# Optimization experiments

Measured on AMD Instinct MI355X. Metric: run time of the kernel, lower is better.

## Reference

```python
import jax, jax.numpy as jnp
import numpy as np

D = 256  # in_channels == out_channels -> output_proj is Identity


def setup_inputs() -> dict:
    key = jax.random.key(0)
    ks = jax.random.split(key, 7)
    B, N = 4, 4096
    s = 1.0 / np.sqrt(D)
    return {
        "x": jax.random.normal(ks[0], (B, N, D), dtype=jnp.float32),
        "Wk": jax.random.normal(ks[1], (D, D), dtype=jnp.float32) * s,
        "bk": jax.random.normal(ks[2], (D,), dtype=jnp.float32) * 0.01,
        "Wq": jax.random.normal(ks[3], (D, D), dtype=jnp.float32) * s,
        "bq": jax.random.normal(ks[4], (D,), dtype=jnp.float32) * 0.01,
        "Wv": jax.random.normal(ks[5], (D, D), dtype=jnp.float32) * s,
        "bv": jax.random.normal(ks[6], (D,), dtype=jnp.float32) * 0.01,
    }


def reference(x, Wk, bk, Wq, bq, Wv, bv):
    # Linear projections: torch Linear(x) = x @ W.T + b; here W is stored as [in, out]
    keys = jnp.einsum("bnd,de->bne", x, Wk) + bk
    queries = jnp.einsum("bnd,de->bne", x, Wq) + bq
    values = jnp.einsum("bnd,de->bne", x, Wv) + bv
    scale = 1.0 / jnp.sqrt(jnp.float32(D))
    scores = jnp.einsum("bqd,bkd->bqk", queries, keys) * scale  # [B, N, N]
    attn = jax.nn.softmax(scores, axis=-1)
    out = jnp.einsum("bqk,bkd->bqd", attn, values)
    return out
```

## Files before the change

kernel.cpp:

```cpp
#include <hip/hip_runtime.h>
#include <hip/hip_bf16.h>


typedef __attribute__((ext_vector_type(8))) short bf16x8;
typedef __attribute__((ext_vector_type(4))) float f32x4;

__device__ __forceinline__ float b2f(ushort u){
  union { uint i; float f; } v; v.i = ((uint)u) << 16; return v.f;
}
__device__ __forceinline__ ushort f2b(float f){
  union { float f; uint i; } v; v.f = f;
  uint i = v.i;
  return (ushort)((i + 0x7FFFu + ((i >> 16) & 1u)) >> 16);
}
__device__ __forceinline__ uint pack2(float a, float b){
  return (uint)f2b(a) | ((uint)f2b(b) << 16);
}

#define Q_SCALE 0.0901684400555602f
#define FIXED_M 16.0f

__global__ __launch_bounds__(256) void transpose_w_kernel(
    const float* __restrict__ Wk, const float* __restrict__ Wq,
    const float* __restrict__ Wv, ushort* __restrict__ Wt){
  __shared__ ushort t[64][72];
  const float* src = (blockIdx.y == 0) ? Wk : (blockIdx.y == 1) ? Wq : Wv;
  ushort* dst = Wt + blockIdx.y * 65536;
  int tile = blockIdx.x;
  int tr = tile >> 2, tc = tile & 3;
  int tid = threadIdx.x;
  for (int i = tid; i < 1024; i += 256){
    int r = i >> 4, ch = i & 15;
    float4 f = *(const float4*)(src + (tr*64 + r)*256 + tc*64 + ch*4);
    uint2 u; u.x = pack2(f.x, f.y); u.y = pack2(f.z, f.w);
    *(uint2*)&t[r][ch*4] = u;
  }
  __syncthreads();
  for (int i = tid; i < 2048; i += 256){
    int c = i >> 5, r2 = (i & 31)*2;
    uint v = (uint)t[r2][c] | ((uint)t[r2+1][c] << 16);
    *(uint*)(dst + (tc*64 + c)*256 + tr*64 + r2) = v;
  }
}

__global__ __launch_bounds__(256) void proj_kernel(
    const float* __restrict__ x, const ushort* __restrict__ Wt,
    const float* __restrict__ bK, const float* __restrict__ bQ,
    const float* __restrict__ bV,
    ushort* __restrict__ Ko, ushort* __restrict__ Qo, ushort* __restrict__ Vt){
  __shared__ ushort xs[64][264];
  __shared__ ushort wt[16][264];
  int my = blockIdx.y;
  int n0 = blockIdx.x * 64;
  const ushort* wsrc = Wt + my*65536;
  const float* bias  = (my==0) ? bK : (my==1) ? bQ : bV;

  int tid = threadIdx.x;
  int lane = tid & 63, w = tid >> 6, quad = lane >> 4, l16 = lane & 15;

  for (int i = tid; i < 4096; i += 256){
    int r = i >> 6, ch = i & 63;
    float4 f = *(const float4*)(x + (size_t)(n0 + r)*256 + ch*4);
    uint2 u; u.x = pack2(f.x, f.y); u.y = pack2(f.z, f.w);
    *(uint2*)&xs[r][ch*4] = u;
  }
  __syncthreads();

  bf16x8 afr[8];
  #pragma unroll
  for (int ks = 0; ks < 8; ks++)
    afr[ks] = *(const bf16x8*)&xs[w*16 + l16][ks*32 + quad*8];

  for (int nt = 0; nt < 16; nt++){
    __syncthreads();
    for (int i = tid; i < 512; i += 256){
      int r = i >> 5, ch = i & 31;
      *(uint4*)&wt[r][ch*8] = *(const uint4*)(wsrc + (nt*16 + r)*256 + ch*8);
    }
    __syncthreads();
    f32x4 acc = {0.f, 0.f, 0.f, 0.f};
    #pragma unroll
    for (int ks = 0; ks < 8; ks++){
      bf16x8 bfr = *(const bf16x8*)&wt[l16][ks*32 + quad*8];
      acc = __builtin_amdgcn_mfma_f32_16x16x32_bf16(afr[ks], bfr, acc, 0, 0, 0);
    }
    int e = nt*16 + l16;
    float bv = bias[e];
    if (my == 2){
      int b  = n0 >> 12;
      int nl = (n0 & 4095) + w*16 + quad*4;
      ushort* vb = Vt + (size_t)b*1048576 + (size_t)e*4096 + nl;
      #pragma unroll
      for (int r = 0; r < 4; r++) vb[r] = f2b(acc[r] + bv);
    } else {
      float scale = (my==1) ? Q_SCALE : 1.0f;
      ushort* out = (my==0) ? Ko : Qo;
      #pragma unroll
      for (int r = 0; r < 4; r++){
        int row = n0 + w*16 + quad*4 + r;
        out[(size_t)row*256 + e] = f2b((acc[r] + bv) * scale);
      }
    }
  }
}

__global__ __launch_bounds__(256, 2) void attn_kernel(
    const ushort* __restrict__ Q, const ushort* __restrict__ K,
    const ushort* __restrict__ Vt,
    float* __restrict__ O0, ushort* __restrict__ Obf, float* __restrict__ lp){
  __shared__ ushort Ks[32][264];
  __shared__ ushort Vs[256][40];
  __shared__ ushort Ps[128][40];

  int bx   = blockIdx.x;
  int bh   = bx & 15;
  int b    = bh >> 2;
  int half = bh & 3;
  int qt   = bx >> 4;
  int tid = threadIdx.x, lane = tid & 63, w = tid >> 6;
  int quad = lane >> 4, l16 = lane & 15;

  const ushort* Qb = Q  + (size_t)(b*4096 + qt*128)*256;
  const ushort* Kb = K  + (size_t)b*4096*256;
  const ushort* Vb = Vt + (size_t)b*256*4096;

  bf16x8 qf[2][8];
  #pragma unroll
  for (int s = 0; s < 2; s++)
    #pragma unroll
    for (int ks = 0; ks < 8; ks++)
      qf[s][ks] = *(const bf16x8*)(Qb + (size_t)(w*32 + s*16 + l16)*256 + ks*32 + quad*8);

  f32x4 of[2][16];
  #pragma unroll
  for (int s = 0; s < 2; s++)
    #pragma unroll
    for (int dt = 0; dt < 16; dt++) of[s][dt] = (f32x4){0.f, 0.f, 0.f, 0.f};
  float l_i[2][4];
  #pragma unroll
  for (int s = 0; s < 2; s++)
    #pragma unroll
    for (int r = 0; r < 4; r++) l_i[s][r] = 0.f;

  int kt0 = half * 32;
  for (int kt = kt0; kt < kt0 + 32; kt++){
    __syncthreads();
    for (int i = tid; i < 1024; i += 256){
      int r = i >> 5, ch = i & 31;
      *(uint4*)&Ks[r][ch*8] = *(const uint4*)(Kb + (size_t)(kt*32 + r)*256 + ch*8);
    }
    for (int i = tid; i < 1024; i += 256){
      int d = i >> 2, ch = i & 3;
      *(uint4*)&Vs[d][ch*8] = *(const uint4*)(Vb + (size_t)d*4096 + kt*32 + ch*8);
    }
    __syncthreads();

    f32x4 sf[2][2];
    #pragma unroll
    for (int s = 0; s < 2; s++)
      #pragma unroll
      for (int nt = 0; nt < 2; nt++) sf[s][nt] = (f32x4){0.f, 0.f, 0.f, 0.f};
    #pragma unroll
    for (int nt = 0; nt < 2; nt++)
      #pragma unroll
      for (int ks = 0; ks < 8; ks++){
        bf16x8 bfr = *(const bf16x8*)&Ks[nt*16 + l16][ks*32 + quad*8];
        sf[0][nt] = __builtin_amdgcn_mfma_f32_16x16x32_bf16(qf[0][ks], bfr, sf[0][nt], 0,0,0);
        sf[1][nt] = __builtin_amdgcn_mfma_f32_16x16x32_bf16(qf[1][ks], bfr, sf[1][nt], 0,0,0);
      }

    #pragma unroll
    for (int s = 0; s < 2; s++){
      #pragma unroll
      for (int r = 0; r < 4; r++){
        float p0 = exp2f(sf[s][0][r] - FIXED_M);
        float p1 = exp2f(sf[s][1][r] - FIXED_M);
        l_i[s][r] += p0 + p1;
        Ps[w*32 + s*16 + quad*4 + r][l16]      = f2b(p0);
        Ps[w*32 + s*16 + quad*4 + r][16 + l16] = f2b(p1);
      }
    }
    __threadfence_block();

    bf16x8 pf0 = *(const bf16x8*)&Ps[w*32 +      l16][quad*8];
    bf16x8 pf1 = *(const bf16x8*)&Ps[w*32 + 16 + l16][quad*8];
    #pragma unroll
    for (int dt = 0; dt < 16; dt++){
      bf16x8 vf = *(const bf16x8*)&Vs[dt*16 + l16][quad*8];
      of[0][dt] = __builtin_amdgcn_mfma_f32_16x16x32_bf16(pf0, vf, of[0][dt], 0, 0, 0);
      of[1][dt] = __builtin_amdgcn_mfma_f32_16x16x32_bf16(pf1, vf, of[1][dt], 0, 0, 0);
    }
  }

  #pragma unroll
  for (int s = 0; s < 2; s++)
    #pragma unroll
    for (int r = 0; r < 4; r++){
      float rs = l_i[s][r];
      #pragma unroll
      for (int msk = 1; msk < 16; msk <<= 1) rs += __shfl_xor(rs, msk, 16);
      l_i[s][r] = rs;
    }

  #pragma unroll
  for (int s = 0; s < 2; s++){
    int gq0 = b*4096 + qt*128 + w*32 + s*16 + quad*4;
    if (l16 == 0){
      #pragma unroll
      for (int r = 0; r < 4; r++)
        lp[(size_t)half*16384 + gq0 + r] = l_i[s][r];
    }
    if (half == 0){
      #pragma unroll
      for (int dt = 0; dt < 16; dt++)
        #pragma unroll
        for (int r = 0; r < 4; r++)
          O0[(size_t)(gq0 + r)*256 + dt*16 + l16] = of[s][dt][r];
    } else {
      ushort* Oh = Obf + (size_t)(half - 1)*16384*256;
      #pragma unroll
      for (int dt = 0; dt < 16; dt++)
        #pragma unroll
        for (int r = 0; r < 4; r++)
          Oh[(size_t)(gq0 + r)*256 + dt*16 + l16] = f2b(of[s][dt][r]);
    }
  }
}

__global__ __launch_bounds__(256) void merge_kernel(
    float* __restrict__ O0, const ushort* __restrict__ Obf,
    const float* __restrict__ lp){
  int t   = blockIdx.x*256 + threadIdx.x;
  int row = t >> 6;
  int c   = (t & 63) * 4;
  float den = lp[row] + lp[16384 + row] + lp[2*16384 + row] + lp[3*16384 + row];
  float rden = 1.0f / den;
  size_t idx = (size_t)row*256 + c;
  float4 acc = *(float4*)&O0[idx];
  #pragma unroll
  for (int h = 1; h < 4; h++){
    ushort4 oh = *(const ushort4*)&Obf[(size_t)(h-1)*16384*256 + idx];
    acc.x += b2f(oh.x); acc.y += b2f(oh.y);
    acc.z += b2f(oh.z); acc.w += b2f(oh.w);
  }
  acc.x *= rden; acc.y *= rden; acc.z *= rden; acc.w *= rden;
  *(float4*)&O0[idx] = acc;
}

extern "C" void kernel_launch(void* const* d_in, const int* in_sizes, int n_in,
                              void* d_out, int out_size, void* d_ws, size_t ws_size,
                              hipStream_t stream){
  const float* x  = (const float*)d_in[0];
  const float* Wk = (const float*)d_in[1];
  const float* bk = (const float*)d_in[2];
  const float* Wq = (const float*)d_in[3];
  const float* bq = (const float*)d_in[4];
  const float* Wv = (const float*)d_in[5];
  const float* bv = (const float*)d_in[6];

  char* ws = (char*)d_ws;
  ushort* Wt  = (ushort*)(ws);
  ushort* Qb  = (ushort*)(ws + (size_t)1*(1u<<20));
  ushort* Kb  = (ushort*)(ws + (size_t)10*(1u<<20));
  ushort* Vtb = (ushort*)(ws + (size_t)19*(1u<<20));
  ushort* Obf = (ushort*)(ws + (size_t)28*(1u<<20));
  float*  lp  = (float*)(ws + (size_t)54*(1u<<20));

  hipLaunchKernelGGL(transpose_w_kernel, dim3(16, 3), dim3(256), 0, stream,
                     Wk, Wq, Wv, Wt);
  hipLaunchKernelGGL(proj_kernel, dim3(256, 3), dim3(256), 0, stream,
                     x, Wt, bk, bq, bv, Kb, Qb, Vtb);
  hipLaunchKernelGGL(attn_kernel, dim3(512), dim3(256), 0, stream,
                     Qb, Kb, Vtb, (float*)d_out, Obf, lp);
  hipLaunchKernelGGL(merge_kernel, dim3(4096), dim3(256), 0, stream,
                     (float*)d_out, Obf, lp);
}
```

Baseline: 237.8 us.

## Split attention KV range six ways, raise occupancy, read proj weights from global

The key range of the attention kernel is now split across six blocks per query tile instead of four. The grid grows to 768 blocks and launch bounds are raised to three blocks per CU, which should fill the 256-CU device more evenly. The projection kernel drops its shared-memory weight staging and the two barriers per tile, reading B fragments straight from global memory instead. The cost is more partial outputs to write and merge, more register pressure under the tighter launch bound, and uncoalesced or repeated weight reads in the projection.

```diff
diff --git a/kernel.cpp b/kernel.cpp
--- a/kernel.cpp
+++ b/kernel.cpp
@@ -19,6 +19,7 @@
 
 #define Q_SCALE 0.0901684400555602f
 #define FIXED_M 16.0f
+#define NSPLIT  6
 
 __global__ __launch_bounds__(256) void transpose_w_kernel(
     const float* __restrict__ Wk, const float* __restrict__ Wq,
@@ -49,7 +50,6 @@
     const float* __restrict__ bV,
     ushort* __restrict__ Ko, ushort* __restrict__ Qo, ushort* __restrict__ Vt){
   __shared__ ushort xs[64][264];
-  __shared__ ushort wt[16][264];
   int my = blockIdx.y;
   int n0 = blockIdx.x * 64;
   const ushort* wsrc = Wt + my*65536;
@@ -72,16 +72,10 @@
     afr[ks] = *(const bf16x8*)&xs[w*16 + l16][ks*32 + quad*8];
 
   for (int nt = 0; nt < 16; nt++){
-    __syncthreads();
-    for (int i = tid; i < 512; i += 256){
-      int r = i >> 5, ch = i & 31;
-      *(uint4*)&wt[r][ch*8] = *(const uint4*)(wsrc + (nt*16 + r)*256 + ch*8);
-    }
-    __syncthreads();
     f32x4 acc = {0.f, 0.f, 0.f, 0.f};
     #pragma unroll
     for (int ks = 0; ks < 8; ks++){
-      bf16x8 bfr = *(const bf16x8*)&wt[l16][ks*32 + quad*8];
+      bf16x8 bfr = *(const bf16x8*)(wsrc + (size_t)(nt*16 + l16)*256 + ks*32 + quad*8);
       acc = __builtin_amdgcn_mfma_f32_16x16x32_bf16(afr[ks], bfr, acc, 0, 0, 0);
     }
     int e = nt*16 + l16;
@@ -104,7 +98,7 @@
   }
 }
 
-__global__ __launch_bounds__(256, 2) void attn_kernel(
+__global__ __launch_bounds__(256, 3) void attn_kernel(
     const ushort* __restrict__ Q, const ushort* __restrict__ K,
     const ushort* __restrict__ Vt,
     float* __restrict__ O0, ushort* __restrict__ Obf, float* __restrict__ lp){
@@ -113,10 +107,10 @@
   __shared__ ushort Ps[128][40];
 
   int bx   = blockIdx.x;
-  int bh   = bx & 15;
-  int b    = bh >> 2;
-  int half = bh & 3;
-  int qt   = bx >> 4;
+  int bh   = bx % 24;
+  int b    = bh / NSPLIT;
+  int h    = bh % NSPLIT;
+  int qt   = bx / 24;
   int tid = threadIdx.x, lane = tid & 63, w = tid >> 6;
   int quad = lane >> 4, l16 = lane & 15;
 
@@ -142,8 +136,8 @@
     #pragma unroll
     for (int r = 0; r < 4; r++) l_i[s][r] = 0.f;
 
-  int kt0 = half * 32;
-  for (int kt = kt0; kt < kt0 + 32; kt++){
+  int kt0 = (h*128)/NSPLIT, kt1 = ((h+1)*128)/NSPLIT;
+  for (int kt = kt0; kt < kt1; kt++){
     __syncthreads();
     for (int i = tid; i < 1024; i += 256){
       int r = i >> 5, ch = i & 31;
@@ -208,16 +202,16 @@
     if (l16 == 0){
       #pragma unroll
       for (int r = 0; r < 4; r++)
-        lp[(size_t)half*16384 + gq0 + r] = l_i[s][r];
-    }
-    if (half == 0){
+        lp[(size_t)h*16384 + gq0 + r] = l_i[s][r];
+    }
+    if (h == 0){
       #pragma unroll
       for (int dt = 0; dt < 16; dt++)
         #pragma unroll
         for (int r = 0; r < 4; r++)
           O0[(size_t)(gq0 + r)*256 + dt*16 + l16] = of[s][dt][r];
     } else {
-      ushort* Oh = Obf + (size_t)(half - 1)*16384*256;
+      ushort* Oh = Obf + (size_t)(h - 1)*16384*256;
       #pragma unroll
       for (int dt = 0; dt < 16; dt++)
         #pragma unroll
@@ -233,12 +227,14 @@
   int t   = blockIdx.x*256 + threadIdx.x;
   int row = t >> 6;
   int c   = (t & 63) * 4;
-  float den = lp[row] + lp[16384 + row] + lp[2*16384 + row] + lp[3*16384 + row];
+  float den = 0.f;
+  #pragma unroll
+  for (int h = 0; h < NSPLIT; h++) den += lp[(size_t)h*16384 + row];
   float rden = 1.0f / den;
   size_t idx = (size_t)row*256 + c;
   float4 acc = *(float4*)&O0[idx];
   #pragma unroll
-  for (int h = 1; h < 4; h++){
+  for (int h = 1; h < NSPLIT; h++){
     ushort4 oh = *(const ushort4*)&Obf[(size_t)(h-1)*16384*256 + idx];
     acc.x += b2f(oh.x); acc.y += b2f(oh.y);
     acc.z += b2f(oh.z); acc.w += b2f(oh.w);
@@ -261,16 +257,16 @@
   char* ws = (char*)d_ws;
   ushort* Wt  = (ushort*)(ws);
   ushort* Qb  = (ushort*)(ws + (size_t)1*(1u<<20));
-  ushort* Kb  = (ushort*)(ws + (size_t)10*(1u<<20));
-  ushort* Vtb = (ushort*)(ws + (size_t)19*(1u<<20));
-  ushort* Obf = (ushort*)(ws + (size_t)28*(1u<<20));
-  float*  lp  = (float*)(ws + (size_t)54*(1u<<20));
+  ushort* Kb  = (ushort*)(ws + (size_t)9*(1u<<20));
+  ushort* Vtb = (ushort*)(ws + (size_t)17*(1u<<20));
+  ushort* Obf = (ushort*)(ws + (size_t)25*(1u<<20));
+  float*  lp  = (float*)(ws + (size_t)65*(1u<<20));
 
   hipLaunchKernelGGL(transpose_w_kernel, dim3(16, 3), dim3(256), 0, stream,
                      Wk, Wq, Wv, Wt);
   hipLaunchKernelGGL(proj_kernel, dim3(256, 3), dim3(256), 0, stream,
                      x, Wt, bk, bq, bv, Kb, Qb, Vtb);
-  hipLaunchKernelGGL(attn_kernel, dim3(512), dim3(256), 0, stream,
+  hipLaunchKernelGGL(attn_kernel, dim3(768), dim3(256), 0, stream,
                      Qb, Kb, Vtb, (float*)d_out, Obf, lp);
   hipLaunchKernelGGL(merge_kernel, dim3(4096), dim3(256), 0, stream,
                      (float*)d_out, Obf, lp);
```

New measurement: 638.7 us. 2.69x slower.
